# Kernel optimization log

Hardware: AMD Instinct MI355X
Metric: run time of the kernel (lower is better)

The kernel has to match this reference:

```python
import jax, jax.numpy as jnp
import numpy as np
import math

B, NQ, NK, D, H = 4, 2048, 2048, 1024, 8
EPS = 1e-5


def _layernorm(x, g, b):
    mu = jnp.mean(x, axis=-1, keepdims=True)
    var = jnp.mean(jnp.square(x - mu), axis=-1, keepdims=True)
    return (x - mu) * jax.lax.rsqrt(var + EPS) * g + b


def setup_inputs() -> dict:
    key = jax.random.key(0)
    ks = jax.random.split(key, 12)
    s = 0.02
    return {
        "q": jax.random.normal(ks[0], (B, NQ, D), jnp.float32),
        "k": jax.random.normal(ks[1], (B, NK, D), jnp.float32),
        "v": jax.random.normal(ks[2], (B, NK, D), jnp.float32),
        "mask": jax.random.randint(ks[3], (B, NK), 0, 2).astype(bool),
        "Wq": jax.random.normal(ks[4], (D, D), jnp.float32) * s,
        "Wk": jax.random.normal(ks[5], (D, D), jnp.float32) * s,
        "Wv": jax.random.normal(ks[6], (D, D), jnp.float32) * s,
        "Wout": jax.random.normal(ks[7], (D, D), jnp.float32) * s,
        "bout": jnp.zeros((D,), jnp.float32),
        "g1": jnp.ones((D,), jnp.float32),
        "b1": jnp.zeros((D,), jnp.float32),
        "g2": jnp.ones((D,), jnp.float32),
        "b2": jnp.zeros((D,), jnp.float32),
    }


def reference(q, k, v, mask, Wq, Wk, Wv, Wout, bout, g1, b1, g2, b2):
    Dh = D // H
    qp = q @ Wq.T  # [B,NQ,D]
    kp = k @ Wk.T  # [B,NK,D]
    vp = v @ Wv.T  # [B,NK,D]
    # scatter: chunk last dim into H heads, cat along batch == reshape to heads
    qh = qp.reshape(B, NQ, H, Dh)
    kh = kp.reshape(B, NK, H, Dh)
    vh = vp.reshape(B, NK, H, Dh)
    # NOTE: original scales by sqrt(dim_out), not sqrt(head_dim)
    logits = jnp.einsum("bqhd,bkhd->bhqk", qh, kh) / math.sqrt(D)
    logits = jnp.where(mask[:, None, None, :], -jnp.inf, logits)
    A = jax.nn.softmax(logits, axis=-1)
    A = jnp.where(jnp.isnan(A), 0.0, A)  # rows fully masked -> 0
    att = jnp.einsum("bhqk,bkhd->bqhd", A, vh).reshape(B, NQ, D)
    out = _layernorm(qp + att, g1, b1)
    out = _layernorm(out + jax.nn.relu(out @ Wout.T + bout), g2, b2)
    return out
```

## Files before the change

kernel.cpp:

```cpp
#include <hip/hip_runtime.h>


typedef __attribute__((ext_vector_type(4))) float f32x4;
typedef __attribute__((ext_vector_type(16))) float f32x16;
typedef __attribute__((ext_vector_type(8))) short s16x8;
typedef __attribute__((ext_vector_type(4))) short s16x4;
typedef __attribute__((ext_vector_type(2))) unsigned int u32x2;

__device__ __forceinline__ unsigned short f2bf(float f) {
  union { float f; unsigned u; } x; x.f = f;
  unsigned r = x.u + 0x7fffu + ((x.u >> 16) & 1u);
  return (unsigned short)(r >> 16);
}
__device__ __forceinline__ float bf2f(unsigned short h) {
  union { unsigned u; float f; } x; x.u = ((unsigned)h) << 16;
  return x.f;
}

__device__ __forceinline__ void gload_lds16(const void* g, void* l) {
  __builtin_amdgcn_global_load_lds(
      (const __attribute__((address_space(1))) unsigned int*)g,
      (__attribute__((address_space(3))) unsigned int*)l, 16, 0, 0);
}

__device__ __forceinline__ unsigned lds_off(const void* p) {
  return (unsigned)(size_t)(const __attribute__((address_space(3))) void*)p;
}

__global__ __launch_bounds__(256) void cvt_multi(
    const float* __restrict__ s0, const float* __restrict__ s1,
    const float* __restrict__ s2, const float* __restrict__ s3,
    unsigned short* __restrict__ d0, unsigned short* __restrict__ d1,
    unsigned short* __restrict__ d2, unsigned short* __restrict__ d3,
    int n4) {
  const int by = blockIdx.y;
  const float* s = by == 0 ? s0 : by == 1 ? s1 : by == 2 ? s2 : s3;
  unsigned short* d = by == 0 ? d0 : by == 1 ? d1 : by == 2 ? d2 : d3;
  int i = blockIdx.x * blockDim.x + threadIdx.x;
  if (i >= n4) return;
  float4 f = reinterpret_cast<const float4*>(s)[i];
  s16x4 o;
  o[0] = (short)f2bf(f.x); o[1] = (short)f2bf(f.y);
  o[2] = (short)f2bf(f.z); o[3] = (short)f2bf(f.w);
  reinterpret_cast<s16x4*>(d)[i] = o;
}

template<int RELU_BIAS>
__global__ __launch_bounds__(256) void gemm_bt(
    const unsigned short* __restrict__ A, const unsigned short* __restrict__ B,
    unsigned short* __restrict__ C, const float* __restrict__ bias,
    int M, int N, int K) {
  __shared__ __align__(16) unsigned short As[128 * 32];
  __shared__ __align__(16) unsigned short Bs[128 * 32];
  const int tid = threadIdx.x;
  const int lane = tid & 63;
  const int w = tid >> 6;
  const int brow = blockIdx.x * 128;
  const int bcol = blockIdx.y * 128;
  const int wr = (w >> 1) * 64;
  const int wc = (w & 1) * 64;

  f32x4 acc[4][4] = {};

  const int srow = w * 32 + (lane >> 2);
  const int scol = (lane & 3) * 8;
  const int rfrag = lane & 15;
  const int kfrag = (lane >> 4) * 8;

  for (int k0 = 0; k0 < K; k0 += 32) {
    __syncthreads();
#pragma unroll
    for (int j = 0; j < 2; ++j) {
      const unsigned short* ga = A + (size_t)(brow + srow + j * 16) * K + k0 + scol;
      gload_lds16(ga, As + (w * 1024 + j * 512));
      const unsigned short* gb = B + (size_t)(bcol + srow + j * 16) * K + k0 + scol;
      gload_lds16(gb, Bs + (w * 1024 + j * 512));
    }
    asm volatile("s_waitcnt vmcnt(0)" ::: "memory");
    __syncthreads();
    s16x8 a[4], b[4];
#pragma unroll
    for (int m = 0; m < 4; ++m)
      a[m] = *(const s16x8*)(As + (wr + m * 16 + rfrag) * 32 + kfrag);
#pragma unroll
    for (int n = 0; n < 4; ++n)
      b[n] = *(const s16x8*)(Bs + (wc + n * 16 + rfrag) * 32 + kfrag);
#pragma unroll
    for (int m = 0; m < 4; ++m)
#pragma unroll
      for (int n = 0; n < 4; ++n)
        acc[m][n] = __builtin_amdgcn_mfma_f32_16x16x32_bf16(a[m], b[n], acc[m][n], 0, 0, 0);
  }

  const int crow = brow + wr + ((lane >> 4) * 4);
  const int ccol = bcol + wc + (lane & 15);
  float bv[4];
  if (RELU_BIAS) {
#pragma unroll
    for (int n = 0; n < 4; ++n) bv[n] = bias[ccol + n * 16];
  }
#pragma unroll
  for (int m = 0; m < 4; ++m)
#pragma unroll
    for (int n = 0; n < 4; ++n)
#pragma unroll
      for (int r = 0; r < 4; ++r) {
        float vv = acc[m][n][r];
        if (RELU_BIAS) vv = fmaxf(vv + bv[n], 0.f);
        C[(size_t)(crow + m * 16 + r) * N + ccol + n * 16] = f2bf(vv);
      }
}

__global__ __launch_bounds__(256) void gemm_proj3(
    const unsigned short* __restrict__ A0, const unsigned short* __restrict__ A1,
    const unsigned short* __restrict__ A2, const unsigned short* __restrict__ B0,
    const unsigned short* __restrict__ B1, const unsigned short* __restrict__ B2,
    unsigned short* __restrict__ C0, unsigned short* __restrict__ C1,
    unsigned short* __restrict__ C2, int M, int N, int K) {
  const int z = blockIdx.z;
  const unsigned short* __restrict__ A = z == 0 ? A0 : z == 1 ? A1 : A2;
  const unsigned short* __restrict__ B = z == 0 ? B0 : z == 1 ? B1 : B2;
  unsigned short* __restrict__ C = z == 0 ? C0 : z == 1 ? C1 : C2;

  __shared__ __align__(16) unsigned short As[128 * 32];
  __shared__ __align__(16) unsigned short Bs[128 * 32];
  const int tid = threadIdx.x;
  const int lane = tid & 63;
  const int w = tid >> 6;
  const int brow = blockIdx.x * 128;
  const int bcol = blockIdx.y * 128;
  const int wr = (w >> 1) * 64;
  const int wc = (w & 1) * 64;

  f32x4 acc[4][4] = {};

  const int srow = w * 32 + (lane >> 2);
  const int scol = (lane & 3) * 8;
  const int rfrag = lane & 15;
  const int kfrag = (lane >> 4) * 8;

  for (int k0 = 0; k0 < K; k0 += 32) {
    __syncthreads();
#pragma unroll
    for (int j = 0; j < 2; ++j) {
      const unsigned short* ga = A + (size_t)(brow + srow + j * 16) * K + k0 + scol;
      gload_lds16(ga, As + (w * 1024 + j * 512));
      const unsigned short* gb = B + (size_t)(bcol + srow + j * 16) * K + k0 + scol;
      gload_lds16(gb, Bs + (w * 1024 + j * 512));
    }
    asm volatile("s_waitcnt vmcnt(0)" ::: "memory");
    __syncthreads();
    s16x8 a[4], b[4];
#pragma unroll
    for (int m = 0; m < 4; ++m)
      a[m] = *(const s16x8*)(As + (wr + m * 16 + rfrag) * 32 + kfrag);
#pragma unroll
    for (int n = 0; n < 4; ++n)
      b[n] = *(const s16x8*)(Bs + (wc + n * 16 + rfrag) * 32 + kfrag);
#pragma unroll
    for (int m = 0; m < 4; ++m)
#pragma unroll
      for (int n = 0; n < 4; ++n)
        acc[m][n] = __builtin_amdgcn_mfma_f32_16x16x32_bf16(a[m], b[n], acc[m][n], 0, 0, 0);
  }

  const int crow = brow + wr + ((lane >> 4) * 4);
  const int ccol = bcol + wc + (lane & 15);
#pragma unroll
  for (int m = 0; m < 4; ++m)
#pragma unroll
    for (int n = 0; n < 4; ++n)
#pragma unroll
      for (int r = 0; r < 4; ++r)
        C[(size_t)(crow + m * 16 + r) * N + ccol + n * 16] = f2bf(acc[m][n][r]);
}

__global__ __launch_bounds__(256, 2) void attn_fused(
    const unsigned short* __restrict__ Qp, const unsigned short* __restrict__ Kp,
    const unsigned short* __restrict__ Vp, const int* __restrict__ mask,
    unsigned short* __restrict__ Att) {
  constexpr int DD = 1024, NK = 2048;
  __shared__ __align__(16) unsigned short lds[24576];
  __shared__ __align__(16) float smaskF[2048];
  unsigned short* Ks = lds;
  unsigned short* Vs = lds + 8192;

  const int tid = threadIdx.x, lane = tid & 63, w = tid >> 6;
  const int quad = lane >> 4, lq = lane & 15;
  const int hi = lane >> 5, q5 = lane & 31;
  const int L = blockIdx.x;
  const int bh = (L & 7) * 4 + (L >> 7);
  const int qt = (L >> 3) & 15;
  const int b = bh >> 3, h = bh & 7;
  const int q0 = qt * 128;
  const unsigned short* Qbase = Qp + ((size_t)b * 2048 + q0) * DD + h * 128;
  const unsigned short* Kbase = Kp + (size_t)b * 2048 * DD + h * 128;
  const unsigned short* Vbase = Vp + (size_t)b * 2048 * DD + h * 128;
  char* PLw = (char*)(lds + 16384 + w * 2048);

#pragma unroll
  for (int j = 0; j < 8; ++j) {
    int row = w * 32 + j * 4 + quad;
    const unsigned short* g = Qbase + (size_t)row * DD + lq * 8;
    gload_lds16(g, lds + w * 4096 + j * 512);
  }
  asm volatile("s_waitcnt vmcnt(0)" ::: "memory");
  __syncthreads();
  s16x8 qf[8];
#pragma unroll
  for (int ds = 0; ds < 8; ++ds)
    qf[ds] = *(const s16x8*)(lds + (w * 32 + q5) * 128 + ds * 16 + hi * 8);

  {
    const int4* mp = (const int4*)(mask + b * NK);
    int4 m0 = mp[tid];
    int4 m1 = mp[tid + 256];
    f32x4 w0, w1;
    w0[0] = m0.x ? -1e30f : 0.f; w0[1] = m0.y ? -1e30f : 0.f;
    w0[2] = m0.z ? -1e30f : 0.f; w0[3] = m0.w ? -1e30f : 0.f;
    w1[0] = m1.x ? -1e30f : 0.f; w1[1] = m1.y ? -1e30f : 0.f;
    w1[2] = m1.z ? -1e30f : 0.f; w1[3] = m1.w ? -1e30f : 0.f;
    *(f32x4*)(smaskF + 4 * tid) = w0;
    *(f32x4*)(smaskF + 4 * (tid + 256)) = w1;
  }

  const unsigned vb0 = lds_off(Vs);
  const int swzq = (q5 & 7) << 4;

  f32x16 o[4] = {};
  float mrow = -1e30f, lrow = 0.f;

  for (int kt = 0; kt < NK / 64; ++kt) {
    const int k0 = kt * 64;
    __syncthreads();
#pragma unroll
    for (int j = 0; j < 4; ++j) {
      int row = w * 16 + j * 4 + quad;
      int cb = lq * 16;
      int cbs = cb ^ ((row & 7) << 4);
      const unsigned short* g = Kbase + (size_t)(k0 + row) * DD + (cbs >> 1);
      gload_lds16(g, Ks + w * 2048 + j * 512);
    }
#pragma unroll
    for (int it = 0; it < 4; ++it) {
      int s = w * 256 + it * 64 + lane;
      int kk = ((s >> 6) << 2) | ((s >> 1) & 3);
      int dd = (((s >> 3) & 7) << 4) | ((s & 1) << 3);
      const unsigned short* g = Vbase + (size_t)(k0 + kk) * DD + dd;
      gload_lds16(g, Vs + (size_t)(w * 256 + it * 64) * 8);
    }
    asm volatile("s_waitcnt vmcnt(0)" ::: "memory");
    __syncthreads();

    f32x16 acc0 = {}, acc1 = {};
    __builtin_amdgcn_s_setprio(1);
#pragma unroll
    for (int ds = 0; ds < 8; ++ds) {
      int cbs = (ds * 32 + hi * 16) ^ swzq;
      s16x8 kf0 = *(const s16x8*)((const char*)Ks + q5 * 256 + cbs);
      s16x8 kf1 = *(const s16x8*)((const char*)Ks + (q5 + 32) * 256 + cbs);
      acc0 = __builtin_amdgcn_mfma_f32_32x32x16_bf16(kf0, qf[ds], acc0, 0, 0, 0);
      acc1 = __builtin_amdgcn_mfma_f32_32x32x16_bf16(kf1, qf[ds], acc1, 0, 0, 0);
    }
    __builtin_amdgcn_s_setprio(0);

    float sv0[16], sv1[16];
#pragma unroll
    for (int g2 = 0; g2 < 4; ++g2) {
      f32x4 m0 = *(const f32x4*)(smaskF + k0 + g2 * 8 + hi * 4);
      f32x4 m1 = *(const f32x4*)(smaskF + k0 + 32 + g2 * 8 + hi * 4);
#pragma unroll
      for (int j2 = 0; j2 < 4; ++j2) {
        sv0[g2 * 4 + j2] = fmaf(acc0[g2 * 4 + j2], 0.03125f, m0[j2]);
        sv1[g2 * 4 + j2] = fmaf(acc1[g2 * 4 + j2], 0.03125f, m1[j2]);
      }
    }

    float tm = fmaxf(sv0[0], sv1[0]);
#pragma unroll
    for (int r = 1; r < 16; ++r) tm = fmaxf(tm, fmaxf(sv0[r], sv1[r]));
    tm = fmaxf(tm, __shfl_xor(tm, 32, 64));
    const bool up = !__all(tm - mrow <= 8.f);
    float al = 1.f;
    if (up) {
      float mn = fmaxf(mrow, tm);
      al = __expf(mrow - mn);
      mrow = mn;
    }
    float rs = 0.f;
#pragma unroll
    for (int g2 = 0; g2 < 4; ++g2) {
      {
        float p0 = __expf(sv0[g2 * 4 + 0] - mrow);
        float p1 = __expf(sv0[g2 * 4 + 1] - mrow);
        float p2 = __expf(sv0[g2 * 4 + 2] - mrow);
        float p3 = __expf(sv0[g2 * 4 + 3] - mrow);
        rs += (p0 + p1) + (p2 + p3);
        unsigned lo, hi2;
        asm("v_cvt_pk_bf16_f32 %0, %1, %2" : "=v"(lo) : "v"(p0), "v"(p1));
        asm("v_cvt_pk_bf16_f32 %0, %1, %2" : "=v"(hi2) : "v"(p2), "v"(p3));
        u32x2 pk; pk[0] = lo; pk[1] = hi2;
        *(u32x2*)(PLw + ((q5 * 128 + g2 * 16 + hi * 8) ^ swzq)) = pk;
      }
      {
        float p0 = __expf(sv1[g2 * 4 + 0] - mrow);
        float p1 = __expf(sv1[g2 * 4 + 1] - mrow);
        float p2 = __expf(sv1[g2 * 4 + 2] - mrow);
        float p3 = __expf(sv1[g2 * 4 + 3] - mrow);
        rs += (p0 + p1) + (p2 + p3);
        unsigned lo, hi2;
        asm("v_cvt_pk_bf16_f32 %0, %1, %2" : "=v"(lo) : "v"(p0), "v"(p1));
        asm("v_cvt_pk_bf16_f32 %0, %1, %2" : "=v"(hi2) : "v"(p2), "v"(p3));
        u32x2 pk; pk[0] = lo; pk[1] = hi2;
        *(u32x2*)(PLw + ((q5 * 128 + 64 + g2 * 16 + hi * 8) ^ swzq)) = pk;
      }
    }
    rs += __shfl_xor(rs, 32, 64);
    lrow = lrow * al + rs;
    if (up) {
#pragma unroll
      for (int reg = 0; reg < 16; ++reg) {
        float alo = __shfl(al, (reg & 3) + 8 * (reg >> 2) + 4 * hi, 64);
#pragma unroll
        for (int db = 0; db < 4; ++db) o[db][reg] *= alo;
      }
    }

    s16x8 pa[4];
#pragma unroll
    for (int kb2 = 0; kb2 < 4; ++kb2)
      pa[kb2] = *(const s16x8*)(
          PLw + ((q5 * 128 + kb2 * 32 + hi * 16) ^ swzq));
#pragma unroll
    for (int db = 0; db < 4; ++db) {
      s16x4 vlo[4], vhi[4];
#pragma unroll
      for (int kb2 = 0; kb2 < 4; ++kb2) {
        const unsigned va = vb0 + (kb2 * 4 + hi * 2) * 1024 +
                            (db * 2 + (quad & 1)) * 128 + lq * 8;
        asm volatile("ds_read_b64_tr_b16 %0, %2\n\t"
                     "ds_read_b64_tr_b16 %1, %2 offset:1024"
                     : "=&v"(vlo[kb2]), "=&v"(vhi[kb2])
                     : "v"(va)
                     : "memory");
      }
      asm volatile("s_waitcnt lgkmcnt(0)" ::: "memory");
      __builtin_amdgcn_sched_barrier(0);
      __builtin_amdgcn_s_setprio(1);
#pragma unroll
      for (int kb2 = 0; kb2 < 4; ++kb2) {
        s16x8 vv;
#pragma unroll
        for (int j = 0; j < 4; ++j) { vv[j] = vlo[kb2][j]; vv[4 + j] = vhi[kb2][j]; }
        o[db] = __builtin_amdgcn_mfma_f32_32x32x16_bf16(pa[kb2], vv, o[db], 0, 0, 0);
      }
      __builtin_amdgcn_s_setprio(0);
    }
  }

  float inv = (mrow <= -1e29f || lrow <= 0.f) ? 0.f : 1.f / lrow;
#pragma unroll
  for (int reg = 0; reg < 16; ++reg) {
    const int rown = (reg & 3) + 8 * (reg >> 2) + 4 * hi;
    float invo = __shfl(inv, rown, 64);
    const int q = q0 + w * 32 + rown;
#pragma unroll
    for (int db = 0; db < 4; ++db) {
      Att[((size_t)b * 2048 + q) * DD + h * 128 + db * 32 + q5] =
          f2bf(o[db][reg] * invo);
    }
  }
}

template<int OUT_F32>
__global__ __launch_bounds__(256) void add_ln(
    const unsigned short* __restrict__ X, const unsigned short* __restrict__ Y,
    const float* __restrict__ gam, const float* __restrict__ bet,
    void* __restrict__ out) {
  const int row = blockIdx.x;
  const int tid = threadIdx.x;
  const int lane = tid & 63, w = tid >> 6;
  __shared__ float rbuf[8];
  const size_t base = (size_t)row * 1024 + tid * 4;
  s16x4 xa = *(const s16x4*)(X + base);
  s16x4 yb = *(const s16x4*)(Y + base);
  float x[4];
  float s1 = 0.f, s2 = 0.f;
#pragma unroll
  for (int j = 0; j < 4; ++j) {
    x[j] = bf2f((unsigned short)xa[j]) + bf2f((unsigned short)yb[j]);
    s1 += x[j];
    s2 += x[j] * x[j];
  }
#pragma unroll
  for (int d = 1; d < 64; d <<= 1) {
    s1 += __shfl_xor(s1, d, 64);
    s2 += __shfl_xor(s2, d, 64);
  }
  if (lane == 0) { rbuf[w] = s1; rbuf[4 + w] = s2; }
  __syncthreads();
  float t1 = rbuf[0] + rbuf[1] + rbuf[2] + rbuf[3];
  float t2 = rbuf[4] + rbuf[5] + rbuf[6] + rbuf[7];
  float mu = t1 * (1.f / 1024.f);
  float var = t2 * (1.f / 1024.f) - mu * mu;
  float rstd = rsqrtf(fmaxf(var, 0.f) + 1e-5f);
  float4 g4 = *(const float4*)(gam + tid * 4);
  float4 b4 = *(const float4*)(bet + tid * 4);
  float gg[4] = {g4.x, g4.y, g4.z, g4.w};
  float bb[4] = {b4.x, b4.y, b4.z, b4.w};
  if (OUT_F32) {
    float4 o4;
    o4.x = (x[0] - mu) * rstd * gg[0] + bb[0];
    o4.y = (x[1] - mu) * rstd * gg[1] + bb[1];
    o4.z = (x[2] - mu) * rstd * gg[2] + bb[2];
    o4.w = (x[3] - mu) * rstd * gg[3] + bb[3];
    *(float4*)((float*)out + base) = o4;
  } else {
    s16x4 o;
#pragma unroll
    for (int j = 0; j < 4; ++j)
      o[j] = (short)f2bf((x[j] - mu) * rstd * gg[j] + bb[j]);
    *(s16x4*)((unsigned short*)out + base) = o;
  }
}

extern "C" void kernel_launch(void* const* d_in, const int* in_sizes, int n_in,
                              void* d_out, int out_size, void* d_ws, size_t ws_size,
                              hipStream_t stream) {
  const float* q  = (const float*)d_in[0];
  const float* k  = (const float*)d_in[1];
  const float* v  = (const float*)d_in[2];
  const int* msk  = (const int*)d_in[3];
  const float* Wq = (const float*)d_in[4];
  const float* Wk = (const float*)d_in[5];
  const float* Wv = (const float*)d_in[6];
  const float* Wo = (const float*)d_in[7];
  const float* bo = (const float*)d_in[8];
  const float* g1 = (const float*)d_in[9];
  const float* b1 = (const float*)d_in[10];
  const float* g2 = (const float*)d_in[11];
  const float* b2 = (const float*)d_in[12];
  float* out = (float*)d_out;

  char* ws = (char*)d_ws;
  const size_t S = (size_t)8192 * 1024 * 2;
  unsigned short* qb  = (unsigned short*)(ws + 0 * S);
  unsigned short* kb  = (unsigned short*)(ws + 1 * S);
  unsigned short* vb  = (unsigned short*)(ws + 2 * S);
  unsigned short* qpb = (unsigned short*)(ws + 3 * S);
  unsigned short* kpb = (unsigned short*)(ws + 4 * S);
  unsigned short* vpb = (unsigned short*)(ws + 5 * S);
  unsigned short* attb = qb;
  unsigned short* h1b  = kb;
  unsigned short* h2b  = vb;
  unsigned short* Wqb = (unsigned short*)(ws + 6 * S);
  unsigned short* Wkb = Wqb + (size_t)1024 * 1024;
  unsigned short* Wvb = Wkb + (size_t)1024 * 1024;
  unsigned short* Wob = Wvb + (size_t)1024 * 1024;

  const int n4big = 8192 * 1024 / 4;
  const int n4w   = 1024 * 1024 / 4;
  cvt_multi<<<dim3(8192, 3), 256, 0, stream>>>(q, k, v, v, qb, kb, vb, vb, n4big);
  cvt_multi<<<dim3(1024, 4), 256, 0, stream>>>(Wq, Wk, Wv, Wo, Wqb, Wkb, Wvb, Wob, n4w);

  gemm_proj3<<<dim3(64, 8, 3), 256, 0, stream>>>(
      qb, kb, vb, Wqb, Wkb, Wvb, qpb, kpb, vpb, 8192, 1024, 1024);

  attn_fused<<<512, 256, 0, stream>>>(qpb, kpb, vpb, msk, attb);

  add_ln<0><<<8192, 256, 0, stream>>>(qpb, attb, g1, b1, (void*)h1b);
  gemm_bt<1><<<dim3(64, 8), 256, 0, stream>>>(h1b, Wob, h2b, bo, 8192, 1024, 1024);
  add_ln<1><<<8192, 256, 0, stream>>>(h1b, h2b, g2, b2, (void*)out);
}
```

Baseline: 240.1 us.

## Double-buffer K/V tiles in attention and read mask from global per tile

Result: slower. 253.8 us (+5.7%).

```diff
diff --git a/kernel.cpp b/kernel.cpp
--- a/kernel.cpp
+++ b/kernel.cpp
@@ -180,10 +180,7 @@
     const unsigned short* __restrict__ Vp, const int* __restrict__ mask,
     unsigned short* __restrict__ Att) {
   constexpr int DD = 1024, NK = 2048;
-  __shared__ __align__(16) unsigned short lds[24576];
-  __shared__ __align__(16) float smaskF[2048];
-  unsigned short* Ks = lds;
-  unsigned short* Vs = lds + 8192;
+  __shared__ __align__(16) unsigned short lds[40960];
 
   const int tid = threadIdx.x, lane = tid & 63, w = tid >> 6;
   const int quad = lane >> 4, lq = lane & 15;
@@ -196,7 +193,7 @@
   const unsigned short* Qbase = Qp + ((size_t)b * 2048 + q0) * DD + h * 128;
   const unsigned short* Kbase = Kp + (size_t)b * 2048 * DD + h * 128;
   const unsigned short* Vbase = Vp + (size_t)b * 2048 * DD + h * 128;
-  char* PLw = (char*)(lds + 16384 + w * 2048);
+  char* PLw = (char*)(lds + 32768 + w * 2048);
 
 #pragma unroll
   for (int j = 0; j < 8; ++j) {
@@ -211,54 +208,63 @@
   for (int ds = 0; ds < 8; ++ds)
     qf[ds] = *(const s16x8*)(lds + (w * 32 + q5) * 128 + ds * 16 + hi * 8);
 
-  {
-    const int4* mp = (const int4*)(mask + b * NK);
-    int4 m0 = mp[tid];
-    int4 m1 = mp[tid + 256];
-    f32x4 w0, w1;
-    w0[0] = m0.x ? -1e30f : 0.f; w0[1] = m0.y ? -1e30f : 0.f;
-    w0[2] = m0.z ? -1e30f : 0.f; w0[3] = m0.w ? -1e30f : 0.f;
-    w1[0] = m1.x ? -1e30f : 0.f; w1[1] = m1.y ? -1e30f : 0.f;
-    w1[2] = m1.z ? -1e30f : 0.f; w1[3] = m1.w ? -1e30f : 0.f;
-    *(f32x4*)(smaskF + 4 * tid) = w0;
-    *(f32x4*)(smaskF + 4 * (tid + 256)) = w1;
-  }
-
-  const unsigned vb0 = lds_off(Vs);
-  const int swzq = (q5 & 7) << 4;
-
-  f32x16 o[4] = {};
-  float mrow = -1e30f, lrow = 0.f;
-
-  for (int kt = 0; kt < NK / 64; ++kt) {
-    const int k0 = kt * 64;
-    __syncthreads();
+  auto stageK = [&](int t, int bsel) {
+    const int kk0 = t * 64;
 #pragma unroll
     for (int j = 0; j < 4; ++j) {
       int row = w * 16 + j * 4 + quad;
       int cb = lq * 16;
       int cbs = cb ^ ((row & 7) << 4);
-      const unsigned short* g = Kbase + (size_t)(k0 + row) * DD + (cbs >> 1);
-      gload_lds16(g, Ks + w * 2048 + j * 512);
-    }
+      const unsigned short* g = Kbase + (size_t)(kk0 + row) * DD + (cbs >> 1);
+      gload_lds16(g, lds + bsel * 8192 + w * 2048 + j * 512);
+    }
+  };
+  auto stageV = [&](int t, int bsel) {
+    const int kk0 = t * 64;
 #pragma unroll
     for (int it = 0; it < 4; ++it) {
       int s = w * 256 + it * 64 + lane;
       int kk = ((s >> 6) << 2) | ((s >> 1) & 3);
       int dd = (((s >> 3) & 7) << 4) | ((s & 1) << 3);
-      const unsigned short* g = Vbase + (size_t)(k0 + kk) * DD + dd;
-      gload_lds16(g, Vs + (size_t)(w * 256 + it * 64) * 8);
-    }
-    asm volatile("s_waitcnt vmcnt(0)" ::: "memory");
+      const unsigned short* g = Vbase + (size_t)(kk0 + kk) * DD + dd;
+      gload_lds16(g, lds + 16384 + bsel * 8192 + w * 2048 + it * 512);
+    }
+  };
+
+  __syncthreads();
+  stageK(0, 0);
+  stageV(0, 0);
+
+  const unsigned vb00 = lds_off(lds + 16384);
+  const int swzq = (q5 & 7) << 4;
+  const int4* mrowp = (const int4*)(mask + b * NK);
+
+  f32x16 o[4] = {};
+  float mrow = -1e30f, lrow = 0.f;
+
+  for (int kt = 0; kt < NK / 64; ++kt) {
+    const int cur = kt & 1;
     __syncthreads();
+    int4 mq0[4], mq1[4];
+#pragma unroll
+    for (int g2 = 0; g2 < 4; ++g2) {
+      mq0[g2] = mrowp[kt * 16 + g2 * 2 + hi];
+      mq1[g2] = mrowp[kt * 16 + 8 + g2 * 2 + hi];
+    }
+    if (kt < NK / 64 - 1) {
+      stageK(kt + 1, cur ^ 1);
+      stageV(kt + 1, cur ^ 1);
+    }
+    const char* Kc = (const char*)lds + cur * 16384;
+    const unsigned vbase = vb00 + cur * 16384;
 
     f32x16 acc0 = {}, acc1 = {};
     __builtin_amdgcn_s_setprio(1);
 #pragma unroll
     for (int ds = 0; ds < 8; ++ds) {
       int cbs = (ds * 32 + hi * 16) ^ swzq;
-      s16x8 kf0 = *(const s16x8*)((const char*)Ks + q5 * 256 + cbs);
-      s16x8 kf1 = *(const s16x8*)((const char*)Ks + (q5 + 32) * 256 + cbs);
+      s16x8 kf0 = *(const s16x8*)(Kc + q5 * 256 + cbs);
+      s16x8 kf1 = *(const s16x8*)(Kc + (q5 + 32) * 256 + cbs);
       acc0 = __builtin_amdgcn_mfma_f32_32x32x16_bf16(kf0, qf[ds], acc0, 0, 0, 0);
       acc1 = __builtin_amdgcn_mfma_f32_32x32x16_bf16(kf1, qf[ds], acc1, 0, 0, 0);
     }
@@ -267,12 +273,15 @@
     float sv0[16], sv1[16];
 #pragma unroll
     for (int g2 = 0; g2 < 4; ++g2) {
-      f32x4 m0 = *(const f32x4*)(smaskF + k0 + g2 * 8 + hi * 4);
-      f32x4 m1 = *(const f32x4*)(smaskF + k0 + 32 + g2 * 8 + hi * 4);
+      f32x4 ma0, ma1;
+      ma0[0] = mq0[g2].x ? -1e30f : 0.f; ma0[1] = mq0[g2].y ? -1e30f : 0.f;
+      ma0[2] = mq0[g2].z ? -1e30f : 0.f; ma0[3] = mq0[g2].w ? -1e30f : 0.f;
+      ma1[0] = mq1[g2].x ? -1e30f : 0.f; ma1[1] = mq1[g2].y ? -1e30f : 0.f;
+      ma1[2] = mq1[g2].z ? -1e30f : 0.f; ma1[3] = mq1[g2].w ? -1e30f : 0.f;
 #pragma unroll
       for (int j2 = 0; j2 < 4; ++j2) {
-        sv0[g2 * 4 + j2] = fmaf(acc0[g2 * 4 + j2], 0.03125f, m0[j2]);
-        sv1[g2 * 4 + j2] = fmaf(acc1[g2 * 4 + j2], 0.03125f, m1[j2]);
+        sv0[g2 * 4 + j2] = fmaf(acc0[g2 * 4 + j2], 0.03125f, ma0[j2]);
+        sv1[g2 * 4 + j2] = fmaf(acc1[g2 * 4 + j2], 0.03125f, ma1[j2]);
       }
     }
 
@@ -336,7 +345,7 @@
       s16x4 vlo[4], vhi[4];
 #pragma unroll
       for (int kb2 = 0; kb2 < 4; ++kb2) {
-        const unsigned va = vb0 + (kb2 * 4 + hi * 2) * 1024 +
+        const unsigned va = vbase + (kb2 * 4 + hi * 2) * 1024 +
                             (db * 2 + (quad & 1)) * 128 + lq * 8;
         asm volatile("ds_read_b64_tr_b16 %0, %2\n\t"
                      "ds_read_b64_tr_b16 %1, %2 offset:1024"
```
